# Optimization experiments

Hardware: AMD Instinct MI355X
Metric: run time of the kernel (lower is better)

## Reference

```python
import jax, jax.numpy as jnp
import numpy as np

N, L, H, D, NCLS = 8192, 1024, 512, 256, 2


def setup_inputs() -> dict:
    key = jax.random.key(0)
    ks = jax.random.split(key, 11)
    s = 0.02  # xavier-ish init scale
    return {
        "x": jax.random.normal(ks[0], (N, L), jnp.float32),
        "W_fc": jax.random.normal(ks[1], (L, H), jnp.float32) * s,
        "b_fc": jnp.zeros((H,), jnp.float32),
        "W_a": jax.random.normal(ks[2], (H, D), jnp.float32) * s,
        "b_a": jnp.zeros((D,), jnp.float32),
        "W_b": jax.random.normal(ks[3], (H, D), jnp.float32) * s,
        "b_b": jnp.zeros((D,), jnp.float32),
        "W_c": jax.random.normal(ks[4], (D, 1), jnp.float32) * s,
        "b_c": jnp.zeros((1,), jnp.float32),
        "W_cls": jax.random.normal(ks[5], (H, NCLS), jnp.float32) * s,
        "b_cls": jnp.zeros((NCLS,), jnp.float32),
    }


def reference(x, W_fc, b_fc, W_a, b_a, W_b, b_b, W_c, b_c, W_cls, b_cls):
    n = x.shape[0]
    # fc: Linear + ReLU (dropout p=0, eval)
    h = jax.nn.relu(x @ W_fc + b_fc)                      # [N, 512]
    # gated attention net (Attn_Net_Gated, n_classes=1)
    a = jnp.tanh(h @ W_a + b_a)                           # [N, 256]
    b = jax.nn.sigmoid(h @ W_b + b_b)                     # [N, 256]
    scores = ((a * b) @ W_c + b_c)[:, 0]                  # [N] diagonal scores
    # A_raw: the original's wasteful CxNxN diagonal matrix (C=1)
    idx = jnp.arange(n)
    A_raw = jnp.zeros((1, n, n), x.dtype).at[0, idx, idx].set(scores)
    # bag_forward: softmax over all N*N entries (N^2 - N zeros off-diagonal),
    # then M = (A @ h).sum(dim=1). Closed form, numerically stable:
    m = jnp.maximum(jnp.max(scores), jnp.zeros((), x.dtype))
    e = jnp.exp(scores - m)                               # diag exp terms
    e0 = jnp.exp(-m)                                      # off-diag exp(0 - m)
    Z = jnp.sum(e) + (n * n - n) * e0
    s = e / Z                                             # softmaxed diagonal
    # row_i @ h = s_i*h_i + (1/Z)*sum_{j!=i} h_j ; sum over i:
    M = s @ h + ((n - 1) * e0 / Z) * jnp.sum(h, axis=0)   # [512]
    logits = M @ W_cls + b_cls                            # [2]
    return (logits[None, :], A_raw)
```

## Files before the change

kernel.cpp:

```cpp
#include <hip/hip_runtime.h>
#include <stdint.h>

#define NROWS 8192
#define LDIM  1024
#define HDIM  512
#define DDIM  256

typedef __attribute__((ext_vector_type(8))) short short8;
typedef __attribute__((ext_vector_type(4))) float f32x4;
typedef __attribute__((ext_vector_type(4))) unsigned int u32x4;

typedef __attribute__((address_space(3))) unsigned int lds_uint;
typedef const __attribute__((address_space(1))) unsigned int glob_uint;

#define ZC_TOTAL 16777215L
#define ZC_MEGA  12582911L
#define ZC_G1    2621440L
#define ZC_G2    1572864L
#define ZB_MEGA  6144
#define ZB_G1    1280
#define ZB_G2    768

__device__ __forceinline__ void llds16(const void* g, void* l) {
  __builtin_amdgcn_global_load_lds((glob_uint*)g, (lds_uint*)l, 16, 0, 0);
}

__device__ __forceinline__ unsigned short f2bf(float f) {
  union { float f; unsigned int u; } c; c.f = f;
  unsigned int u = c.u;
  unsigned int r = (u + 0x7fffu + ((u >> 16) & 1u)) >> 16;
  return (unsigned short)r;
}

__device__ __forceinline__ float bfbits2f(unsigned int hi16) {
  union { unsigned int u; float f; } c; c.u = hi16;
  return c.f;
}

__device__ __forceinline__ void zero_duty(u32x4* __restrict__ out16, long zstart, long zcount,
                                          int zblk, int tid) {
  long b0 = zstart + (long)zblk * 2048;
  long lim = zstart + zcount;
  long b1 = b0 + 2048 < lim ? b0 + 2048 : lim;
  u32x4 z = {0u, 0u, 0u, 0u};
  for (long i = b0 + tid; i < b1; i += 256) out16[i] = z;
}

__global__ __launch_bounds__(256) void mega_bw_kernel(const float* __restrict__ x,
                                                      const float* __restrict__ Wfc,
                                                      const float* __restrict__ Wa,
                                                      const float* __restrict__ Wb,
                                                      unsigned short* __restrict__ xb,
                                                      unsigned short* __restrict__ WfcT,
                                                      unsigned short* __restrict__ WabT,
                                                      float* __restrict__ out) {
  const int bid = blockIdx.x;
  const int tid = threadIdx.x;
  if (bid < ZB_MEGA) {
    zero_duty((u32x4*)(out + 4), 0L, ZC_MEGA, bid, tid);
    if (bid == 0 && tid == 0) {
      out[2] = 0.f; out[3] = 0.f;
      out[67108864] = 0.f; out[67108865] = 0.f;
    }
    return;
  }
  if (bid < ZB_MEGA + 4096) {
    long i = ((long)(bid - ZB_MEGA) * 256 + tid) * 8;
    float4 v0 = *(const float4*)(x + i);
    float4 v1 = *(const float4*)(x + i + 4);
    union { unsigned short s[8]; uint4 u; } o;
    o.s[0] = f2bf(v0.x); o.s[1] = f2bf(v0.y); o.s[2] = f2bf(v0.z); o.s[3] = f2bf(v0.w);
    o.s[4] = f2bf(v1.x); o.s[5] = f2bf(v1.y); o.s[6] = f2bf(v1.z); o.s[7] = f2bf(v1.w);
    *(uint4*)(xb + i) = o.u;
    return;
  }
  int idx = (bid - ZB_MEGA - 4096) * 256 + tid;
  if (idx < 512 * 1024) {
    int n = idx >> 10, k = idx & 1023;
    WfcT[idx] = f2bf(Wfc[k * 512 + n]);
  } else {
    int j = idx - 512 * 1024;
    int n = j >> 9, k = j & 511;
    float v = (n < 256) ? Wa[k * 256 + n] : Wb[k * 256 + (n - 256)];
    WabT[j] = f2bf(v);
  }
}

template <int EPI>
__global__ __launch_bounds__(256) void gemm_bt(const unsigned short* __restrict__ A,
                                               const unsigned short* __restrict__ Bt,
                                               const float* __restrict__ bias,
                                               void* __restrict__ out,
                                               int M, int N, int K,
                                               float* __restrict__ zout, long zstart, long zcount) {
  constexpr int BM = 128, BN = 64, BK = 32;
  __shared__ unsigned short sA[2][BM * BK];
  __shared__ unsigned short sB[2][BN * BK];
  const int tid = threadIdx.x;
  const int nbn = N / BN;
  const int ncomp = (M / BM) * nbn;
  if ((int)blockIdx.x >= ncomp) {
    zero_duty((u32x4*)(zout + 4), zstart, zcount, (int)blockIdx.x - ncomp, tid);
    return;
  }
  const int lane = tid & 63;
  const int wv = tid >> 6;
  const int wm = wv >> 1;
  const int wn = wv & 1;
  const int bm = blockIdx.x / nbn, bn = blockIdx.x % nbn;
  const int row0 = bm * BM, col0 = bn * BN;

  f32x4 acc[4][2] = {};
  const int nk = K / BK;

  auto stage = [&](int buf, int kt) {
#pragma unroll
    for (int r = 0; r < 2; ++r) {
      int c = r * 256 + tid;
      int arow = c >> 2, acb = (c & 3) * 8;
      const unsigned short* g = A + (long)(row0 + arow) * K + kt * BK + acb;
      unsigned short* l = (unsigned short*)&sA[buf][(r * 256 + wv * 64) * 8];
      llds16(g, l);
    }
    {
      int c = tid;
      int brow = c >> 2, bcb = (c & 3) * 8;
      const unsigned short* g = Bt + (long)(col0 + brow) * K + kt * BK + bcb;
      unsigned short* l = (unsigned short*)&sB[buf][(wv * 64) * 8];
      llds16(g, l);
    }
  };

  stage(0, 0);
  __syncthreads();

  for (int kt = 0; kt < nk; ++kt) {
    int cur = kt & 1;
    if (kt + 1 < nk) stage(cur ^ 1, kt + 1);
    const unsigned short* bA = sA[cur];
    const unsigned short* bB = sB[cur];
    short8 af[4], bfr[2];
#pragma unroll
    for (int fm = 0; fm < 4; ++fm)
      af[fm] = *(const short8*)&bA[(wm * 64 + fm * 16 + (lane & 15)) * BK + (lane >> 4) * 8];
#pragma unroll
    for (int fn = 0; fn < 2; ++fn)
      bfr[fn] = *(const short8*)&bB[(wn * 32 + fn * 16 + (lane & 15)) * BK + (lane >> 4) * 8];
#pragma unroll
    for (int fm = 0; fm < 4; ++fm)
#pragma unroll
      for (int fn = 0; fn < 2; ++fn)
        acc[fm][fn] = __builtin_amdgcn_mfma_f32_16x16x32_bf16(af[fm], bfr[fn], acc[fm][fn], 0, 0, 0);
    __syncthreads();
  }

#pragma unroll
  for (int fm = 0; fm < 4; ++fm) {
#pragma unroll
    for (int fn = 0; fn < 2; ++fn) {
#pragma unroll
      for (int i = 0; i < 4; ++i) {
        int row = row0 + wm * 64 + fm * 16 + (lane >> 4) * 4 + i;
        int col = col0 + wn * 32 + fn * 16 + (lane & 15);
        float v = acc[fm][fn][i];
        if (EPI == 0) {
          v += bias[col];
          v = v > 0.f ? v : 0.f;
          ((unsigned short*)out)[(long)row * N + col] = f2bf(v);
        } else {
          ((float*)out)[(long)row * N + col] = v;
        }
      }
    }
  }
}

__global__ __launch_bounds__(256) void score_kernel(const float* __restrict__ t,
                                                    const float* __restrict__ ba,
                                                    const float* __restrict__ bb,
                                                    const float* __restrict__ Wc,
                                                    const float* __restrict__ bc,
                                                    float* __restrict__ scores,
                                                    float* __restrict__ out ) {
  int row = blockIdx.x * 4 + (threadIdx.x >> 6);
  int lane = threadIdx.x & 63;
  const float* tr = t + (long)row * 512;
  float s = 0.f;
#pragma unroll
  for (int j = 0; j < 4; ++j) {
    int d = lane + j * 64;
    float u = tr[d] + ba[d];
    float v = tr[d + 256] + bb[d];
    float av = tanhf(u);
    float bv = 1.f / (1.f + __expf(-v));
    s += av * bv * Wc[d];
  }
#pragma unroll
  for (int off = 32; off; off >>= 1) s += __shfl_down(s, off);
  if (lane == 0) {
    float sc = s + bc[0];
    scores[row] = sc;
    out[2 + (long)row * 8193] = sc;
  }
}

__global__ __launch_bounds__(1024) void reduce_kernel(const float* __restrict__ scores,
                                                      float* __restrict__ w) {
  __shared__ float red[1024];
  int t = threadIdx.x;
  float v[8];
  float mx = -1e30f;
#pragma unroll
  for (int j = 0; j < 8; ++j) { v[j] = scores[t * 8 + j]; mx = fmaxf(mx, v[j]); }
  red[t] = mx; __syncthreads();
  for (int s = 512; s; s >>= 1) { if (t < s) red[t] = fmaxf(red[t], red[t + s]); __syncthreads(); }
  float m = fmaxf(red[0], 0.f);
  __syncthreads();
  float e[8]; float se = 0.f;
#pragma unroll
  for (int j = 0; j < 8; ++j) { e[j] = __expf(v[j] - m); se += e[j]; }
  red[t] = se; __syncthreads();
  for (int s = 512; s; s >>= 1) { if (t < s) red[t] += red[t + s]; __syncthreads(); }
  float e0 = __expf(-m);
  float Z = red[0] + 67100672.0f * e0;
  float c0 = 8191.0f * e0 / Z;
#pragma unroll
  for (int j = 0; j < 8; ++j) w[t * 8 + j] = e[j] / Z + c0;
}

__global__ __launch_bounds__(256) void wsum_kernel(const unsigned short* __restrict__ h,
                                                   const float* __restrict__ w,
                                                   float* __restrict__ part) {
  int b = blockIdx.x;
  int t = threadIdx.x;
  float a0 = 0.f, a1 = 0.f;
  for (int i = b * 128; i < b * 128 + 128; ++i) {
    float wi = w[i];
    unsigned int hv = *(const unsigned int*)&h[(long)i * 512 + t * 2];
    a0 += wi * bfbits2f(hv << 16);
    a1 += wi * bfbits2f(hv & 0xffff0000u);
  }
  part[b * 512 + t * 2] = a0;
  part[b * 512 + t * 2 + 1] = a1;
}

__global__ __launch_bounds__(512) void final_kernel(const float* __restrict__ part,
                                                    const float* __restrict__ Wcls,
                                                    const float* __restrict__ bcls,
                                                    float* __restrict__ out) {
  __shared__ float Msh[512];
  int t = threadIdx.x;
  float s = 0.f;
  for (int b = 0; b < 64; ++b) s += part[b * 512 + t];
  Msh[t] = s;
  __syncthreads();
  if (t < 64) {
    float p0 = 0.f, p1 = 0.f;
    for (int j = t; j < 512; j += 64) { p0 += Msh[j] * Wcls[j * 2]; p1 += Msh[j] * Wcls[j * 2 + 1]; }
#pragma unroll
    for (int off = 32; off; off >>= 1) { p0 += __shfl_down(p0, off); p1 += __shfl_down(p1, off); }
    if (t == 0) { out[0] = p0 + bcls[0]; out[1] = p1 + bcls[1]; }
  }
}

extern "C" void kernel_launch(void* const* d_in, const int* in_sizes, int n_in,
                              void* d_out, int out_size, void* d_ws, size_t ws_size,
                              hipStream_t stream) {
  const float* x    = (const float*)d_in[0];
  const float* Wfc  = (const float*)d_in[1];
  const float* bfc  = (const float*)d_in[2];
  const float* Wa   = (const float*)d_in[3];
  const float* ba   = (const float*)d_in[4];
  const float* Wb   = (const float*)d_in[5];
  const float* bb   = (const float*)d_in[6];
  const float* Wc   = (const float*)d_in[7];
  const float* bc   = (const float*)d_in[8];
  const float* Wcls = (const float*)d_in[9];
  const float* bcls = (const float*)d_in[10];
  float* out = (float*)d_out;
  char* ws = (char*)d_ws;

  unsigned short* xb     = (unsigned short*)(ws + 0);
  unsigned short* WfcT   = (unsigned short*)(ws + 16777216);
  unsigned short* WabT   = (unsigned short*)(ws + 17825792);
  unsigned short* hbuf   = (unsigned short*)(ws + 18350080);
  float*          tbuf   = (float*)(ws + 26738688);
  float*          scores = (float*)(ws + 43515904);
  float*          wbuf   = (float*)(ws + 43548672);
  float*          part   = (float*)(ws + 43581440);

  mega_bw_kernel<<<ZB_MEGA + 4096 + 3072, 256, 0, stream>>>(x, Wfc, Wa, Wb, xb, WfcT, WabT, out);
  gemm_bt<0><<<(NROWS / 128) * (HDIM / 64) + ZB_G1, 256, 0, stream>>>(
      xb, WfcT, bfc, hbuf, NROWS, HDIM, LDIM, out, ZC_MEGA, ZC_G1);
  gemm_bt<1><<<(NROWS / 128) * (HDIM / 64) + ZB_G2, 256, 0, stream>>>(
      hbuf, WabT, nullptr, tbuf, NROWS, HDIM, HDIM, out, ZC_MEGA + ZC_G1, ZC_G2);
  score_kernel<<<NROWS / 4, 256, 0, stream>>>(tbuf, ba, bb, Wc, bc, scores, out);
  reduce_kernel<<<1, 1024, 0, stream>>>(scores, wbuf);
  wsum_kernel<<<64, 256, 0, stream>>>(hbuf, wbuf, part);
  final_kernel<<<1, 512, 0, stream>>>(part, Wcls, bcls, out);
}
```

Before: 122.7 us.

## Widen GEMM tile to 128x128, tile-transpose weights, rebalance zero-fill across kernels

Raises the GEMM block tile from 128x64 to 128x128, so each wave computes a 64x64 region with 4x4 MFMA fragments. This gives more reuse of staged A data per block, with fewer compute blocks in exchange. Weight transposes now go through a padded LDS 32x32 tile, giving coalesced reads and writes in place of strided scalar accesses. The zero-fill of the large A_raw output is split differently across the pre-pass, both GEMMs and the score kernel. Diagonal score writes move to reduce_kernel so they land after the score kernel's zeroing.

Result: faster. 117.4 us (-4.3%).

```diff
diff --git a/kernel.cpp b/kernel.cpp
--- a/kernel.cpp
+++ b/kernel.cpp
@@ -4,7 +4,6 @@
 #define NROWS 8192
 #define LDIM  1024
 #define HDIM  512
-#define DDIM  256
 
 typedef __attribute__((ext_vector_type(8))) short short8;
 typedef __attribute__((ext_vector_type(4))) float f32x4;
@@ -13,13 +12,18 @@
 typedef __attribute__((address_space(3))) unsigned int lds_uint;
 typedef const __attribute__((address_space(1))) unsigned int glob_uint;
 
-#define ZC_TOTAL 16777215L
-#define ZC_MEGA  12582911L
-#define ZC_G1    2621440L
-#define ZC_G2    1572864L
-#define ZB_MEGA  6144
-#define ZB_G1    1280
-#define ZB_G2    768
+#define ZN_TOTAL 16777215L
+#define Z_MEGA_START 0L
+#define Z_MEGA_CNT   6291455L
+#define ZB_MEGA      3072
+#define Z_G1_START   6291455L
+#define Z_G1_CNT     5242880L
+#define ZB_G1        2560
+#define Z_G2_START   11534335L
+#define Z_G2_CNT     3670016L
+#define ZB_G2        1792
+#define Z_SC_START   15204351L
+#define Z_SC_PER     768L
 
 __device__ __forceinline__ void llds16(const void* g, void* l) {
   __builtin_amdgcn_global_load_lds((glob_uint*)g, (lds_uint*)l, 16, 0, 0);
@@ -37,13 +41,9 @@
   return c.f;
 }
 
-__device__ __forceinline__ void zero_duty(u32x4* __restrict__ out16, long zstart, long zcount,
-                                          int zblk, int tid) {
-  long b0 = zstart + (long)zblk * 2048;
-  long lim = zstart + zcount;
-  long b1 = b0 + 2048 < lim ? b0 + 2048 : lim;
+__device__ __forceinline__ void zero_chunks(u32x4* __restrict__ out16, long c0, long c1, int tid) {
   u32x4 z = {0u, 0u, 0u, 0u};
-  for (long i = b0 + tid; i < b1; i += 256) out16[i] = z;
+  for (long i = c0 + tid; i < c1; i += 256) out16[i] = z;
 }
 
 __global__ __launch_bounds__(256) void mega_bw_kernel(const float* __restrict__ x,
@@ -54,10 +54,13 @@
                                                       unsigned short* __restrict__ WfcT,
                                                       unsigned short* __restrict__ WabT,
                                                       float* __restrict__ out) {
+  __shared__ float tile[32][33];
   const int bid = blockIdx.x;
   const int tid = threadIdx.x;
   if (bid < ZB_MEGA) {
-    zero_duty((u32x4*)(out + 4), 0L, ZC_MEGA, bid, tid);
+    long c0 = Z_MEGA_START + (long)bid * 2048;
+    long c1 = c0 + 2048 < Z_MEGA_START + Z_MEGA_CNT ? c0 + 2048 : Z_MEGA_START + Z_MEGA_CNT;
+    zero_chunks((u32x4*)(out + 4), c0, c1, tid);
     if (bid == 0 && tid == 0) {
       out[2] = 0.f; out[3] = 0.f;
       out[67108864] = 0.f; out[67108865] = 0.f;
@@ -74,16 +77,28 @@
     *(uint4*)(xb + i) = o.u;
     return;
   }
-  int idx = (bid - ZB_MEGA - 4096) * 256 + tid;
-  if (idx < 512 * 1024) {
-    int n = idx >> 10, k = idx & 1023;
-    WfcT[idx] = f2bf(Wfc[k * 512 + n]);
+  int tt = bid - (ZB_MEGA + 4096);
+  const float* src; unsigned short* dst; int srcn, dstk, k0, n0;
+  if (tt < 512) {
+    src = Wfc; dst = WfcT; srcn = 512; dstk = 1024;
+    k0 = (tt >> 4) * 32; n0 = (tt & 15) * 32;
+  } else if (tt < 640) {
+    int t2 = tt - 512;
+    src = Wa; dst = WabT; srcn = 256; dstk = 512;
+    k0 = (t2 >> 3) * 32; n0 = (t2 & 7) * 32;
   } else {
-    int j = idx - 512 * 1024;
-    int n = j >> 9, k = j & 511;
-    float v = (n < 256) ? Wa[k * 256 + n] : Wb[k * 256 + (n - 256)];
-    WabT[j] = f2bf(v);
-  }
+    int t2 = tt - 640;
+    src = Wb; dst = WabT + 256 * 512; srcn = 256; dstk = 512;
+    k0 = (t2 >> 3) * 32; n0 = (t2 & 7) * 32;
+  }
+  int r = tid >> 3, c4 = (tid & 7) * 4;
+  float4 v = *(const float4*)(src + (long)(k0 + r) * srcn + n0 + c4);
+  tile[r][c4 + 0] = v.x; tile[r][c4 + 1] = v.y; tile[r][c4 + 2] = v.z; tile[r][c4 + 3] = v.w;
+  __syncthreads();
+  union { unsigned short s[4]; uint2 u; } o;
+#pragma unroll
+  for (int j = 0; j < 4; ++j) o.s[j] = f2bf(tile[c4 + j][r]);
+  *(uint2*)(dst + (long)(n0 + r) * dstk + k0 + c4) = o.u;
 }
 
 template <int EPI>
@@ -93,14 +108,18 @@
                                                void* __restrict__ out,
                                                int M, int N, int K,
                                                float* __restrict__ zout, long zstart, long zcount) {
-  constexpr int BM = 128, BN = 64, BK = 32;
+  constexpr int BM = 128, BN = 128, BK = 32;
   __shared__ unsigned short sA[2][BM * BK];
   __shared__ unsigned short sB[2][BN * BK];
   const int tid = threadIdx.x;
   const int nbn = N / BN;
   const int ncomp = (M / BM) * nbn;
   if ((int)blockIdx.x >= ncomp) {
-    zero_duty((u32x4*)(zout + 4), zstart, zcount, (int)blockIdx.x - ncomp, tid);
+    int zb = (int)blockIdx.x - ncomp;
+    long c0 = zstart + (long)zb * 2048;
+    long lim = zstart + zcount;
+    long c1 = c0 + 2048 < lim ? c0 + 2048 : lim;
+    zero_chunks((u32x4*)(zout + 4), c0, c1, tid);
     return;
   }
   const int lane = tid & 63;
@@ -110,7 +129,7 @@
   const int bm = blockIdx.x / nbn, bn = blockIdx.x % nbn;
   const int row0 = bm * BM, col0 = bn * BN;
 
-  f32x4 acc[4][2] = {};
+  f32x4 acc[4][4] = {};
   const int nk = K / BK;
 
   auto stage = [&](int buf, int kt) {
@@ -122,11 +141,12 @@
       unsigned short* l = (unsigned short*)&sA[buf][(r * 256 + wv * 64) * 8];
       llds16(g, l);
     }
-    {
-      int c = tid;
+#pragma unroll
+    for (int r = 0; r < 2; ++r) {
+      int c = r * 256 + tid;
       int brow = c >> 2, bcb = (c & 3) * 8;
       const unsigned short* g = Bt + (long)(col0 + brow) * K + kt * BK + bcb;
-      unsigned short* l = (unsigned short*)&sB[buf][(wv * 64) * 8];
+      unsigned short* l = (unsigned short*)&sB[buf][(r * 256 + wv * 64) * 8];
       llds16(g, l);
     }
   };
@@ -139,17 +159,17 @@
     if (kt + 1 < nk) stage(cur ^ 1, kt + 1);
     const unsigned short* bA = sA[cur];
     const unsigned short* bB = sB[cur];
-    short8 af[4], bfr[2];
+    short8 af[4], bfr[4];
 #pragma unroll
     for (int fm = 0; fm < 4; ++fm)
       af[fm] = *(const short8*)&bA[(wm * 64 + fm * 16 + (lane & 15)) * BK + (lane >> 4) * 8];
 #pragma unroll
-    for (int fn = 0; fn < 2; ++fn)
-      bfr[fn] = *(const short8*)&bB[(wn * 32 + fn * 16 + (lane & 15)) * BK + (lane >> 4) * 8];
+    for (int fn = 0; fn < 4; ++fn)
+      bfr[fn] = *(const short8*)&bB[(wn * 64 + fn * 16 + (lane & 15)) * BK + (lane >> 4) * 8];
 #pragma unroll
     for (int fm = 0; fm < 4; ++fm)
 #pragma unroll
-      for (int fn = 0; fn < 2; ++fn)
+      for (int fn = 0; fn < 4; ++fn)
         acc[fm][fn] = __builtin_amdgcn_mfma_f32_16x16x32_bf16(af[fm], bfr[fn], acc[fm][fn], 0, 0, 0);
     __syncthreads();
   }
@@ -157,11 +177,11 @@
 #pragma unroll
   for (int fm = 0; fm < 4; ++fm) {
 #pragma unroll
-    for (int fn = 0; fn < 2; ++fn) {
+    for (int fn = 0; fn < 4; ++fn) {
 #pragma unroll
       for (int i = 0; i < 4; ++i) {
         int row = row0 + wm * 64 + fm * 16 + (lane >> 4) * 4 + i;
-        int col = col0 + wn * 32 + fn * 16 + (lane & 15);
+        int col = col0 + wn * 64 + fn * 16 + (lane & 15);
         float v = acc[fm][fn][i];
         if (EPI == 0) {
           v += bias[col];
@@ -182,6 +202,10 @@
                                                     const float* __restrict__ bc,
                                                     float* __restrict__ scores,
                                                     float* __restrict__ out ) {
+  {
+    long c0 = Z_SC_START + (long)blockIdx.x * Z_SC_PER;
+    zero_chunks((u32x4*)(out + 4), c0, c0 + Z_SC_PER, threadIdx.x);
+  }
   int row = blockIdx.x * 4 + (threadIdx.x >> 6);
   int lane = threadIdx.x & 63;
   const float* tr = t + (long)row * 512;
@@ -197,21 +221,20 @@
   }
 #pragma unroll
   for (int off = 32; off; off >>= 1) s += __shfl_down(s, off);
-  if (lane == 0) {
-    float sc = s + bc[0];
-    scores[row] = sc;
-    out[2 + (long)row * 8193] = sc;
-  }
+  if (lane == 0) scores[row] = s + bc[0];
 }
 
 __global__ __launch_bounds__(1024) void reduce_kernel(const float* __restrict__ scores,
-                                                      float* __restrict__ w) {
+                                                      float* __restrict__ w,
+                                                      float* __restrict__ out) {
   __shared__ float red[1024];
   int t = threadIdx.x;
   float v[8];
   float mx = -1e30f;
 #pragma unroll
   for (int j = 0; j < 8; ++j) { v[j] = scores[t * 8 + j]; mx = fmaxf(mx, v[j]); }
+#pragma unroll
+  for (int j = 0; j < 8; ++j) out[2 + 8193L * (t * 8 + j)] = v[j];
   red[t] = mx; __syncthreads();
   for (int s = 512; s; s >>= 1) { if (t < s) red[t] = fmaxf(red[t], red[t + s]); __syncthreads(); }
   float m = fmaxf(red[0], 0.f);
@@ -289,13 +312,13 @@
   float*          wbuf   = (float*)(ws + 43548672);
   float*          part   = (float*)(ws + 43581440);
 
-  mega_bw_kernel<<<ZB_MEGA + 4096 + 3072, 256, 0, stream>>>(x, Wfc, Wa, Wb, xb, WfcT, WabT, out);
-  gemm_bt<0><<<(NROWS / 128) * (HDIM / 64) + ZB_G1, 256, 0, stream>>>(
-      xb, WfcT, bfc, hbuf, NROWS, HDIM, LDIM, out, ZC_MEGA, ZC_G1);
-  gemm_bt<1><<<(NROWS / 128) * (HDIM / 64) + ZB_G2, 256, 0, stream>>>(
-      hbuf, WabT, nullptr, tbuf, NROWS, HDIM, HDIM, out, ZC_MEGA + ZC_G1, ZC_G2);
+  mega_bw_kernel<<<ZB_MEGA + 4096 + 768, 256, 0, stream>>>(x, Wfc, Wa, Wb, xb, WfcT, WabT, out);
+  gemm_bt<0><<<(NROWS / 128) * (HDIM / 128) + ZB_G1, 256, 0, stream>>>(
+      xb, WfcT, bfc, hbuf, NROWS, HDIM, LDIM, out, Z_G1_START, Z_G1_CNT);
+  gemm_bt<1><<<(NROWS / 128) * (HDIM / 128) + ZB_G2, 256, 0, stream>>>(
+      hbuf, WabT, nullptr, tbuf, NROWS, HDIM, HDIM, out, Z_G2_START, Z_G2_CNT);
   score_kernel<<<NROWS / 4, 256, 0, stream>>>(tbuf, ba, bb, Wc, bc, scores, out);
-  reduce_kernel<<<1, 1024, 0, stream>>>(scores, wbuf);
+  reduce_kernel<<<1, 1024, 0, stream>>>(scores, wbuf, out);
   wsum_kernel<<<64, 256, 0, stream>>>(hbuf, wbuf, part);
   final_kernel<<<1, 512, 0, stream>>>(part, Wcls, bcls, out);
 }
```
